# Optimization experiments

Hardware: AMD Instinct MI355X
Metric: run time of the kernel (lower is better)

Reference implementation:

```python
import jax, jax.numpy as jnp
import numpy as np

# ---- constants derived from configs / input sizes ----
H1, W1 = 480, 640
H2, W2 = 480, 640
WINDOW = 0.125      # normalized half-window (config['window_size'])
WG = 16             # window grid resolution per axis
L = 128             # samples along epipolar line (line_search_config)
T_BASE, T_MAX = 1.0, 50.0
NEG = -1e9


def l2norm(x, axis):
    return x / jnp.maximum(jnp.linalg.norm(x, axis=axis, keepdims=True), 1e-12)


def denorm(c_n, h, w):
    # normalized [-1,1] (xy) -> pixel coords, align_corners=True convention
    return jnp.stack([(c_n[..., 0] + 1) * (w - 1) / 2,
                      (c_n[..., 1] + 1) * (h - 1) / 2], -1)


def bilinear_sample(feat, coords_n):
    # feat [b,d,h,w], coords_n [b,n,2] in [-1,1] (xy); bilinear, zero padding
    b, d, h, w = feat.shape
    x = (coords_n[..., 0] + 1) * (w - 1) / 2
    y = (coords_n[..., 1] + 1) * (h - 1) / 2
    x0 = jnp.floor(x); y0 = jnp.floor(y)
    wx1 = x - x0; wx0 = 1 - wx1
    wy1 = y - y0; wy0 = 1 - wy1
    featT = feat.reshape(b, d, h * w).transpose(0, 2, 1)  # [b,hw,d]
    def gather(xi, yi, wgt):
        inb = (xi >= 0) & (xi <= w - 1) & (yi >= 0) & (yi <= h - 1)
        xi_ = jnp.clip(xi, 0, w - 1).astype(jnp.int32)
        yi_ = jnp.clip(yi, 0, h - 1).astype(jnp.int32)
        idx = yi_ * w + xi_
        v = jnp.take_along_axis(featT, idx[..., None], axis=1)  # [b,n,d]
        return v * (wgt * inb)[..., None]
    return (gather(x0, y0, wx0 * wy0) + gather(x0 + 1, y0, wx1 * wy0)
            + gather(x0, y0 + 1, wx0 * wy1) + gather(x0 + 1, y0 + 1, wx1 * wy1))


def soft_expect(corr, coords_n, valid):
    # corr [b,n,L], coords_n [b,n,L,2]; masked soft-argmax + std
    logits = jnp.where(valid, corr, NEG)
    p = jax.nn.softmax(logits, axis=-1)
    mean = jnp.einsum('bnl,bnlc->bnc', p, coords_n)
    var = jnp.einsum('bnl,bnlc->bnc', p, coords_n ** 2) - mean ** 2
    std = jnp.sqrt(jnp.clip(var, 0).sum(-1) + 1e-12)
    return mean, std, p


def epipolar_line_search(coord1_px, Fm, feat1, featmap2, h2, w2):
    # coord1_px [b,n,2] pixels in img1; Fm [b,3,3]; feat1 [b,n,d];
    # featmap2 [b,d,hf,wf] (already temperature * l2-normalized)
    b, n, _ = coord1_px.shape
    p1 = jnp.concatenate([coord1_px, jnp.ones_like(coord1_px[..., :1])], -1)
    line = jnp.einsum('bij,bnj->bni', Fm, p1)  # a x + b y + c = 0 in img2
    a, bb, c = line[..., 0], line[..., 1], line[..., 2]
    eps = 1e-8
    use_x = jnp.abs(bb) >= jnp.abs(a)  # near-horizontal line -> sweep x
    t = jnp.linspace(0.0, 1.0, L)
    xs_h = jnp.broadcast_to(t[None, None, :] * (w2 - 1), (b, n, L))
    ys_h = -(a[..., None] * xs_h + c[..., None]) / jnp.where(jnp.abs(bb) < eps, eps, bb)[..., None]
    ys_v = jnp.broadcast_to(t[None, None, :] * (h2 - 1), (b, n, L))
    xs_v = -(bb[..., None] * ys_v + c[..., None]) / jnp.where(jnp.abs(a) < eps, eps, a)[..., None]
    xs = jnp.where(use_x[..., None], xs_h, xs_v)
    ys = jnp.where(use_x[..., None], ys_h, ys_v)
    valid = (xs >= 0) & (xs <= w2 - 1) & (ys >= 0) & (ys <= h2 - 1)
    degen = (jnp.abs(a) < eps) & (jnp.abs(bb) < eps)
    valid = valid & (~degen[..., None])
    coords_n = jnp.stack([xs / ((w2 - 1) / 2) - 1, ys / ((h2 - 1) / 2) - 1], -1)
    feat_line = bilinear_sample(featmap2, coords_n.reshape(b, n * L, 2)).reshape(b, n, L, -1)
    corr = jnp.einsum('bnd,bnld->bnl', feat1, feat_line)
    mean, std, _ = soft_expect(corr, coords_n, valid)
    valid_kpt = valid.any(-1)
    clamped = jnp.clip(mean, -1 + WINDOW, 1 - WINDOW)  # window fits inside image
    return clamped, mean, valid_kpt, std


def window_expect(feat1, featmap2, center_n):
    b, n, _ = center_n.shape
    off = jnp.linspace(-WINDOW, WINDOW, WG)
    oy, ox = jnp.meshgrid(off, off, indexing='ij')
    offsets = jnp.stack([ox.ravel(), oy.ravel()], -1)            # [WG*WG,2]
    coords_n = center_n[:, :, None, :] + offsets[None, None]    # [b,n,K,2]
    K = WG * WG
    feat_w = bilinear_sample(featmap2, coords_n.reshape(b, n * K, 2)).reshape(b, n, K, -1)
    corr = jnp.einsum('bnd,bnkd->bnk', feat1, feat_w)
    valid = jnp.ones(corr.shape, bool)
    mean, std, p = soft_expect(corr, coords_n, valid)
    return mean, coords_n, std, p


def setup_inputs() -> dict:
    key = jax.random.key(0)
    ks = jax.random.split(key, 6)
    b, d, hf, wf, n = 2, 128, 60, 80, 1024
    xf1 = jax.random.normal(ks[0], (b, d, hf, wf), jnp.float32)
    xf2 = jax.random.normal(ks[1], (b, d, hf, wf), jnp.float32)
    # fundamental-matrix-like magnitudes so epipolar lines cross the image
    scale = jnp.array([[1e-5, 1e-5, 1e-2], [1e-5, 1e-5, 1e-2], [1e-2, 1e-2, 1.0]], jnp.float32)
    F1 = jax.random.normal(ks[2], (b, 3, 3), jnp.float32) * scale
    F2 = jax.random.normal(ks[3], (b, 3, 3), jnp.float32) * scale
    coord1_n = (jax.random.uniform(ks[4], (b, n, 2), jnp.float32) * 2 - 1) * 0.95
    coord2_n = (jax.random.uniform(ks[5], (b, n, 2), jnp.float32) * 2 - 1) * 0.95
    return {"xf1": xf1, "xf2": xf2, "F1": F1, "F2": F2,
            "coord1_n": coord1_n, "coord2_n": coord2_n, "epoch": 10}


def reference(xf1, xf2, F1, F2, coord1_n, coord2_n, epoch):
    temperature = jnp.minimum(jnp.float32(T_BASE + epoch), T_MAX)
    coord1 = denorm(coord1_n, H1, W1)
    coord2 = denorm(coord2_n, H2, W2)
    # loss_distance == 'cos' -> l2-normalize sampled descriptors
    feat1 = l2norm(bilinear_sample(xf1, coord1_n), -1)
    feat2 = l2norm(bilinear_sample(xf2, coord2_n), -1)
    fm2 = temperature * l2norm(xf2, 1)
    fm1 = temperature * l2norm(xf1, 1)
    c1_cl, c1_org_n, valid1, epi_std1 = epipolar_line_search(coord1, F1, feat1, fm2, H2, W2)
    c2_cl, c2_org_n, valid2, epi_std2 = epipolar_line_search(coord2, F2, feat2, fm1, H1, W1)
    feat1c_corloc_org = denorm(c1_org_n, H2, W2)
    f1w_n, _, f1w_std, _ = window_expect(feat1, fm2, c1_cl)
    f2w_n, _, f2w_std, _ = window_expect(feat2, fm1, c2_cl)
    feat1w_corloc = denorm(f1w_n, H2, W2)
    feat2w_corloc = denorm(f2w_n, H1, W1)
    # note: original (faithfully) returns the NORMALIZED coords for image-2 org key
    return (coord1, coord2, feat1w_corloc, feat2w_corloc,
            feat1c_corloc_org, c2_org_n, f1w_std, f2w_std, valid1, valid2)
```

## Files before the change

### kernel.cpp

```cpp
#include <hip/hip_runtime.h>
#include <stdint.h>

namespace {

typedef _Float16 half_t;
typedef _Float16 half2_t __attribute__((ext_vector_type(2)));

constexpr int D    = 128;
constexpr int WFm  = 80;
constexpr int HFm  = 60;
constexpr int NPIX = WFm * HFm;
constexpr int NKPT = 1024;
constexpr int LCX  = 12;
constexpr int LCY  = 10;
constexpr int NLAT = LCX * LCY;

__device__ __forceinline__ float wsum(float v) {
#pragma unroll
  for (int m = 32; m; m >>= 1) v += __shfl_xor(v, m, 64);
  return v;
}
__device__ __forceinline__ float wmax(float v) {
#pragma unroll
  for (int m = 32; m; m >>= 1) v = fmaxf(v, __shfl_xor(v, m, 64));
  return v;
}

__device__ __forceinline__ float dot2acc(uint32_t m, uint32_t f, float acc) {
#if defined(__has_builtin) && __has_builtin(__builtin_amdgcn_fdot2)
  return __builtin_amdgcn_fdot2(__builtin_bit_cast(half2_t, m),
                                __builtin_bit_cast(half2_t, f), acc, false);
#else
  half2_t a = __builtin_bit_cast(half2_t, m);
  half2_t b = __builtin_bit_cast(half2_t, f);
  return acc + (float)a.x * (float)b.x + (float)a.y * (float)b.y;
#endif
}
__device__ __forceinline__ float dot4x2(uint4 m, uint4 f, float acc) {
  acc = dot2acc(m.x, f.x, acc);
  acc = dot2acc(m.y, f.y, acc);
  acc = dot2acc(m.z, f.z, acc);
  acc = dot2acc(m.w, f.w, acc);
  return acc;
}

__global__ __launch_bounds__(256) void prep_kernel(
    const float* __restrict__ xf1, const float* __restrict__ xf2,
    const int* __restrict__ epoch,
    half_t* __restrict__ xf1H, half_t* __restrict__ xf2H,
    float* __restrict__ sc1, float* __restrict__ sc2) {
  __shared__ float tile[32 * 129];
  __shared__ float qSh[8][32];
  __shared__ float sSh[32];

  const int bi   = blockIdx.x;
  const int img  = bi / 300;
  const int rem  = bi % 300;
  const int b    = rem / 150;
  const int p0   = (rem % 150) * 32;
  const int tid  = threadIdx.x;

  const float* src  = img ? xf2 : xf1;
  half_t* dstH      = img ? xf2H : xf1H;
  float* dstS       = img ? sc2 : sc1;
  const float T     = fminf(1.0f + (float)(*epoch), 50.0f);

  const int dc = tid >> 5;
  const int px = tid & 31;
#pragma unroll 4
  for (int it = 0; it < 16; ++it) {
    int d = it * 8 + dc;
    tile[px * 129 + d] = src[((size_t)(b * D + d)) * NPIX + p0 + px];
  }
  __syncthreads();

  {
    float s = 0.f;
    const int d0 = dc * 16;
#pragma unroll 8
    for (int d = 0; d < 16; ++d) {
      float v = tile[px * 129 + d0 + d];
      s += v * v;
    }
    qSh[dc][px] = s;
  }
  __syncthreads();
  if (tid < 32) {
    float s = 0.f;
#pragma unroll
    for (int k = 0; k < 8; ++k) s += qSh[k][tid];
    float sv = T / fmaxf(sqrtf(s), 1e-12f);
    dstS[b * NPIX + p0 + tid] = sv;
    sSh[tid] = sv;
  }
  __syncthreads();

#pragma unroll 4
  for (int it = 0; it < 8; ++it) {
    int idx = it * 256 + tid;
    int lpx = idx >> 6;
    int dp  = idx & 63;
    float s = sSh[lpx];
    half2_t hv;
    hv.x = (half_t)(tile[lpx * 129 + 2 * dp] * s);
    hv.y = (half_t)(tile[lpx * 129 + 2 * dp + 1] * s);
    *reinterpret_cast<half2_t*>(dstH + ((size_t)(b * NPIX + p0 + lpx)) * D + 2 * dp) = hv;
  }
}

__global__ __launch_bounds__(256) void line2win_kernel(
    const half_t* __restrict__ xf1H, const half_t* __restrict__ xf2H,
    const float* __restrict__ sc1, const float* __restrict__ sc2,
    const float* __restrict__ F1, const float* __restrict__ F2,
    const float* __restrict__ c1n, const float* __restrict__ c2n,
    float* __restrict__ out) {
  __shared__ __align__(16) half_t featH[4][D];
  __shared__ float4 sPar[4][2][128];
  __shared__ float corrSh[4][128];
  __shared__ float dm[4][NLAT + 8];

  const int tid  = threadIdx.x;
  const int lane = tid & 63;
  const int wv   = tid >> 6;
  const int w    = blockIdx.x;
  const int xcd  = w & 7;
  const int comb = xcd >> 1;
  const int dir  = comb >> 1;
  const int b    = comb & 1;
  const int n    = ((w >> 3) * 2 + (xcd & 1)) * 4 + wv;
  const int kix  = b * NKPT + n;

  const half_t* srcH = dir ? xf2H : xf1H;
  const float*  ssc  = dir ? sc2 : sc1;
  const half_t* tgtH = dir ? xf1H : xf2H;
  const float*  Fm   = (dir ? F2 : F1) + b * 9;
  const float*  cn   = (dir ? c2n : c1n) + kix * 2;

  const float cnx_in = cn[0], cny_in = cn[1];
  const float px = (cnx_in + 1.f) * 319.5f;
  const float py = (cny_in + 1.f) * 239.5f;

  const float la = Fm[0] * px + Fm[1] * py + Fm[2];
  const float lb = Fm[3] * px + Fm[4] * py + Fm[5];
  const float lc = Fm[6] * px + Fm[7] * py + Fm[8];
  const float eps = 1e-8f;
  const bool  use_x = fabsf(lb) >= fabsf(la);
  const float bden  = (fabsf(lb) < eps) ? eps : lb;
  const float aden  = (fabsf(la) < eps) ? eps : la;
  const float rdenom = 1.f / (use_x ? bden : aden);
  const bool  degen = (fabsf(la) < eps) && (fabsf(lb) < eps);

  const size_t tb = (size_t)b * NPIX * D;

  float f0 = 0.f, f1 = 0.f;
  {
    float xf = (cnx_in + 1.f) * 39.5f;
    float yf = (cny_in + 1.f) * 29.5f;
    float x0 = floorf(xf), y0 = floorf(yf);
    float wx1 = xf - x0, wx0 = 1.f - wx1;
    float wy1 = yf - y0, wy0 = 1.f - wy1;
#pragma unroll
    for (int cyi = 0; cyi < 2; ++cyi)
#pragma unroll
      for (int cxi = 0; cxi < 2; ++cxi) {
        float xi = x0 + (float)cxi, yi = y0 + (float)cyi;
        bool inb = (xi >= 0.f) && (xi <= (float)(WFm - 1)) &&
                   (yi >= 0.f) && (yi <= (float)(HFm - 1));
        float wgt = (cxi ? wx1 : wx0) * (cyi ? wy1 : wy0);
        if (inb && wgt != 0.f) {
          int p = (int)yi * WFm + (int)xi;
          float coef = wgt / ssc[b * NPIX + p];
          half2_t hv = *reinterpret_cast<const half2_t*>(srcH + tb + (size_t)p * D + 2 * lane);
          f0 += coef * (float)hv.x;
          f1 += coef * (float)hv.y;
        }
      }
  }

#pragma unroll
  for (int q = 0; q < 2; ++q) {
    int j = lane + q * 64;
    float tpar = (float)j / 127.0f;
    float xs, ys;
    if (use_x) { xs = tpar * 639.f; ys = -fmaf(la, xs, lc) * rdenom; }
    else       { ys = tpar * 479.f; xs = -fmaf(lb, ys, lc) * rdenom; }
    float xff = fminf(fmaxf(xs * (39.5f / 319.5f), -4.f), 84.f);
    float yff = fminf(fmaxf(ys * (29.5f / 239.5f), -4.f), 64.f);
    float x0f = floorf(xff), y0f = floorf(yff);
    int  x0i = (int)x0f, y0i = (int)y0f;
    float wx1 = xff - x0f, wx0 = 1.f - wx1;
    float wy1 = yff - y0f;
    int  xLow = min(max(x0i, 0), WFm - 2);
    float cL0 = (xLow == x0i) ? wx0 : ((xLow == x0i + 1) ? wx1 : 0.f);
    float cH0 = (xLow + 1 == x0i) ? wx0 : ((xLow + 1 == x0i + 1) ? wx1 : 0.f);
#pragma unroll
    for (int h = 0; h < 2; ++h) {
      int yi = y0i + h;
      bool yin = (yi >= 0) && (yi <= HFm - 1);
      int yc = min(max(yi, 0), HFm - 1);
      float wyh = h ? wy1 : (1.f - wy1);
      float ymul = yin ? wyh : 0.f;
      float4 p4;
      p4.x = __int_as_float(yc * WFm + xLow);
      p4.y = cL0 * ymul;
      p4.z = cH0 * ymul;
      p4.w = 0.f;
      sPar[wv][h][j] = p4;
    }
  }

  const float nrm = wsum(f0 * f0 + f1 * f1);
  const float inv = 1.f / fmaxf(sqrtf(nrm), 1e-12f);
  {
    half2_t hv;
    hv.x = (half_t)(f0 * inv);
    hv.y = (half_t)(f1 * inv);
    *reinterpret_cast<half2_t*>(&featH[wv][2 * lane]) = hv;
  }

  const uint4* fH4 = reinterpret_cast<const uint4*>(featH[wv]);

  {
    const int g = lane >> 4;
    const int s = lane & 7;
    const int h = (lane >> 3) & 1;
    const uint4 fL0 = fH4[s];
    const uint4 fL1 = fH4[8 + s];

    float4 pA = sPar[wv][h][g];
    bool actA = (pA.y != 0.f) || (pA.z != 0.f);
    uint4 a0{}, a1{}, a2{}, a3{};
    if (actA) {
      const uint4* rp = reinterpret_cast<const uint4*>(
          tgtH + tb + (size_t)__float_as_int(pA.x) * D);
      a0 = rp[s]; a1 = rp[8 + s]; a2 = rp[16 + s]; a3 = rp[24 + s];
    }
    float4 pB = sPar[wv][h][4 + g];
    bool actB = (pB.y != 0.f) || (pB.z != 0.f);
    uint4 b0{}, b1{}, b2{}, b3{};
    if (actB) {
      const uint4* rp = reinterpret_cast<const uint4*>(
          tgtH + tb + (size_t)__float_as_int(pB.x) * D);
      b0 = rp[s]; b1 = rp[8 + s]; b2 = rp[16 + s]; b3 = rp[24 + s];
    }

#pragma unroll
    for (int it = 0; it < 32; ++it) {
      float4 pC = {0.f, 0.f, 0.f, 0.f};
      bool actC = false;
      uint4 c0{}, c1{}, c2{}, c3{};
      if (it < 30) {
        pC = sPar[wv][h][(it + 2) * 4 + g];
        actC = (pC.y != 0.f) || (pC.z != 0.f);
        if (actC) {
          const uint4* rp = reinterpret_cast<const uint4*>(
              tgtH + tb + (size_t)__float_as_int(pC.x) * D);
          c0 = rp[s]; c1 = rp[8 + s]; c2 = rp[16 + s]; c3 = rp[24 + s];
        }
      }
      float acc = 0.f;
      if (actA) {
        float accL = dot4x2(a1, fL1, dot4x2(a0, fL0, 0.f));
        float accH = dot4x2(a3, fL1, dot4x2(a2, fL0, 0.f));
        acc = pA.y * accL + pA.z * accH;
      }
      acc += __shfl_xor(acc, 1, 64);
      acc += __shfl_xor(acc, 2, 64);
      acc += __shfl_xor(acc, 4, 64);
      acc += __shfl_xor(acc, 8, 64);
      if ((lane & 15) == 0) corrSh[wv][it * 4 + g] = acc;
      pA = pB; actA = actB; a0 = b0; a1 = b1; a2 = b2; a3 = b3;
      pB = pC; actB = actC; b0 = c0; b1 = c1; b2 = c2; b3 = c3;
    }
  }

  float e0, e1, cx0, cy0, cx1, cy1;
  bool v0, v1;
  {
    float lgt0, lgt1;
#pragma unroll
    for (int q = 0; q < 2; ++q) {
      int j = lane + q * 64;
      float tpar = (float)j / 127.0f;
      float xs, ys;
      if (use_x) { xs = tpar * 639.f; ys = -fmaf(la, xs, lc) * rdenom; }
      else       { ys = tpar * 479.f; xs = -fmaf(lb, ys, lc) * rdenom; }
      bool valid = (xs >= 0.f) && (xs <= 639.f) && (ys >= 0.f) && (ys <= 479.f) && !degen;
      float cxj = xs / 319.5f - 1.f;
      float cyj = ys / 239.5f - 1.f;
      float lg = valid ? corrSh[wv][j] : -1e9f;
      if (q == 0) { v0 = valid; cx0 = cxj; cy0 = cyj; lgt0 = lg; }
      else        { v1 = valid; cx1 = cxj; cy1 = cyj; lgt1 = lg; }
    }
    const float mx = wmax(fmaxf(lgt0, lgt1));
    e0 = expf(lgt0 - mx);
    e1 = expf(lgt1 - mx);
  }
  const float sumE = wsum(e0 + e1);
  const float sumX = wsum(e0 * cx0 + e1 * cx1);
  const float sumY = wsum(e0 * cy0 + e1 * cy1);
  const bool  anyv = __ballot(v0 || v1) != 0ull;
  const float meanx = sumX / sumE;
  const float meany = sumY / sumE;
  const float ccx = fminf(fmaxf(meanx, -0.875f), 0.875f);
  const float ccy = fminf(fmaxf(meany, -0.875f), 0.875f);

  if (lane == 0) {
    float* o_coord = out + dir * 4096 + kix * 2;
    o_coord[0] = px;
    o_coord[1] = py;
    float* o_org = out + 16384 + dir * 4096 + kix * 2;
    if (dir == 0) {
      o_org[0] = (meanx + 1.f) * 319.5f;
      o_org[1] = (meany + 1.f) * 239.5f;
    } else {
      o_org[0] = meanx;
      o_org[1] = meany;
    }
    out[28672 + dir * 2048 + kix] = anyv ? 1.f : 0.f;
  }

  const float xfc2 = (ccx + 1.f) * 39.5f;
  const float yfc2 = (ccy + 1.f) * 29.5f;
  const int xb = (int)floorf(xfc2 - 4.9375f);
  const int yb = (int)floorf(yfc2 - 3.6875f);
  {
    const int s4 = lane & 15;
    const int pp = lane >> 4;
    const uint4 fw = fH4[s4];
    const int x0p = xb + pp, x1p = xb + 4 + pp, x2p = xb + 8 + pp;
    const bool okx0 = x0p <= WFm - 1, okx1 = x1p <= WFm - 1, okx2 = x2p <= WFm - 1;
    const int pc0 = min(x0p, WFm - 1) - xb;
    const int pc1 = min(x1p, WFm - 1) - xb;
    const int pc2 = min(x2p, WFm - 1) - xb;

    const uint4* rpA = reinterpret_cast<const uint4*>(
        tgtH + tb + (size_t)(min(yb, HFm - 1) * WFm + xb) * D);
    uint4 A0 = rpA[pc0 * 16 + s4];
    uint4 A1 = rpA[pc1 * 16 + s4];
    uint4 A2 = rpA[pc2 * 16 + s4];
#pragma unroll
    for (int row = 0; row < LCY; ++row) {
      uint4 B0{}, B1{}, B2{};
      if (row < LCY - 1) {
        int ycl = min(yb + row + 1, HFm - 1);
        const uint4* rpB = reinterpret_cast<const uint4*>(
            tgtH + tb + (size_t)(ycl * WFm + xb) * D);
        B0 = rpB[pc0 * 16 + s4];
        B1 = rpB[pc1 * 16 + s4];
        B2 = rpB[pc2 * 16 + s4];
      }
      bool yok = (yb + row) <= HFm - 1;
      float d0 = dot4x2(A0, fw, 0.f);
      float d1 = dot4x2(A1, fw, 0.f);
      float d2 = dot4x2(A2, fw, 0.f);
#pragma unroll
      for (int m = 1; m <= 8; m <<= 1) {
        d0 += __shfl_xor(d0, m, 64);
        d1 += __shfl_xor(d1, m, 64);
        d2 += __shfl_xor(d2, m, 64);
      }
      if (s4 == 0) {
        dm[wv][row * LCX + pp]     = (yok && okx0) ? d0 : 0.f;
        dm[wv][row * LCX + 4 + pp] = (yok && okx1) ? d1 : 0.f;
        dm[wv][row * LCX + 8 + pp] = (yok && okx2) ? d2 : 0.f;
      }
      A0 = B0; A1 = B1; A2 = B2;
    }
  }

  const float step = 0.25f / 15.f;
  float t0 = 0.f, t1 = 0.f, t2 = 0.f, t3 = 0.f, t4 = 0.f;
#pragma unroll
  for (int q = 0; q < 4; ++q) {
    int k = lane + q * 64;
    float ox = -0.125f + step * (float)(k & 15);
    float oy = -0.125f + step * (float)(k >> 4);
    float kcx = ccx + ox;
    float kcy = ccy + oy;
    float xfw = xfc2 + ox * 39.5f;
    float yfw = yfc2 + oy * 29.5f;
    float xw0 = floorf(xfw), yw0 = floorf(yfw);
    int ix = (int)xw0 - xb;
    int iy = (int)yw0 - yb;
    float wxx1 = xfw - xw0, wxx0 = 1.f - wxx1;
    float wyy1 = yfw - yw0, wyy0 = 1.f - wyy1;
    int i00 = iy * LCX + ix;
    float c00 = dm[wv][i00], c10 = dm[wv][i00 + 1];
    float c01 = dm[wv][i00 + LCX], c11 = dm[wv][i00 + LCX + 1];
    float corr2 = wxx0 * wyy0 * c00 + wxx1 * wyy0 * c10 +
                  wxx0 * wyy1 * c01 + wxx1 * wyy1 * c11;
    float e2 = expf(corr2);
    t0 += e2;
    t1 += e2 * kcx;
    t2 += e2 * kcy;
    t3 += e2 * kcx * kcx;
    t4 += e2 * kcy * kcy;
  }
  t0 = wsum(t0);
  t1 = wsum(t1);
  t2 = wsum(t2);
  t3 = wsum(t3);
  t4 = wsum(t4);
  if (lane == 0) {
    float mwx = t1 / t0;
    float mwy = t2 / t0;
    float vx  = fmaxf(t3 / t0 - mwx * mwx, 0.f);
    float vy  = fmaxf(t4 / t0 - mwy * mwy, 0.f);
    float stdv = sqrtf(vx + vy + 1e-12f);
    float* o_w = out + 8192 + dir * 4096 + kix * 2;
    o_w[0] = (mwx + 1.f) * 319.5f;
    o_w[1] = (mwy + 1.f) * 239.5f;
    out[24576 + dir * 2048 + kix] = stdv;
  }
}

}

extern "C" void kernel_launch(void* const* d_in, const int* in_sizes, int n_in,
                              void* d_out, int out_size, void* d_ws, size_t ws_size,
                              hipStream_t stream) {
  (void)in_sizes; (void)n_in; (void)out_size; (void)ws_size;
  const float* xf1 = (const float*)d_in[0];
  const float* xf2 = (const float*)d_in[1];
  const float* F1  = (const float*)d_in[2];
  const float* F2  = (const float*)d_in[3];
  const float* c1n = (const float*)d_in[4];
  const float* c2n = (const float*)d_in[5];
  const int* epoch = (const int*)d_in[6];

  half_t* xf1H = (half_t*)d_ws;
  half_t* xf2H = xf1H + (size_t)2 * NPIX * D;
  float*  sc1  = (float*)(xf2H + (size_t)2 * NPIX * D);
  float*  sc2  = sc1 + 2 * NPIX;
  float*  out  = (float*)d_out;

  hipLaunchKernelGGL(prep_kernel, dim3(600), dim3(256), 0, stream,
                     xf1, xf2, epoch, xf1H, xf2H, sc1, sc2);
  hipLaunchKernelGGL(line2win_kernel, dim3(1024), dim3(256), 0, stream,
                     xf1H, xf2H, sc1, sc2, F1, F2, c1n, c2n, out);
}
```

Baseline: 37.62 us.

## Split each keypoint's line and window search across two waves per block

Instead of one wavefront handling a whole keypoint (four keypoints per 256-thread block), each keypoint now gets a 128-thread block of two wavefronts. One wave samples and normalises the source descriptor while the other builds the line sample parameters. Both waves then share the 128 line correlations, the window rows and the window expectation samples, with partial sums combined through shared memory. This cuts the serial per-keypoint latency and launches four times as many blocks, at the cost of extra __syncthreads barriers and some duplicated softmax work in both waves.

```diff
diff --git a/kernel.cpp b/kernel.cpp
--- a/kernel.cpp
+++ b/kernel.cpp
@@ -108,26 +108,27 @@
   }
 }
 
-__global__ __launch_bounds__(256) void line2win_kernel(
+__global__ __launch_bounds__(128) void line2win_kernel(
     const half_t* __restrict__ xf1H, const half_t* __restrict__ xf2H,
     const float* __restrict__ sc1, const float* __restrict__ sc2,
     const float* __restrict__ F1, const float* __restrict__ F2,
     const float* __restrict__ c1n, const float* __restrict__ c2n,
     float* __restrict__ out) {
-  __shared__ __align__(16) half_t featH[4][D];
-  __shared__ float4 sPar[4][2][128];
-  __shared__ float corrSh[4][128];
-  __shared__ float dm[4][NLAT + 8];
+  __shared__ __align__(16) half_t featH[D];
+  __shared__ float4 sPar[2][128];
+  __shared__ float corrSh[128];
+  __shared__ float dm[NLAT + 8];
+  __shared__ float pT[2][5];
 
   const int tid  = threadIdx.x;
   const int lane = tid & 63;
-  const int wv   = tid >> 6;
+  const int wvh  = tid >> 6;
   const int w    = blockIdx.x;
   const int xcd  = w & 7;
   const int comb = xcd >> 1;
   const int dir  = comb >> 1;
   const int b    = comb & 1;
-  const int n    = ((w >> 3) * 2 + (xcd & 1)) * 4 + wv;
+  const int n    = (w >> 3) * 2 + (xcd & 1);
   const int kix  = b * NKPT + n;
 
   const half_t* srcH = dir ? xf2H : xf1H;
@@ -152,73 +153,73 @@
 
   const size_t tb = (size_t)b * NPIX * D;
 
-  float f0 = 0.f, f1 = 0.f;
-  {
-    float xf = (cnx_in + 1.f) * 39.5f;
-    float yf = (cny_in + 1.f) * 29.5f;
-    float x0 = floorf(xf), y0 = floorf(yf);
-    float wx1 = xf - x0, wx0 = 1.f - wx1;
-    float wy1 = yf - y0, wy0 = 1.f - wy1;
-#pragma unroll
-    for (int cyi = 0; cyi < 2; ++cyi)
-#pragma unroll
-      for (int cxi = 0; cxi < 2; ++cxi) {
-        float xi = x0 + (float)cxi, yi = y0 + (float)cyi;
-        bool inb = (xi >= 0.f) && (xi <= (float)(WFm - 1)) &&
-                   (yi >= 0.f) && (yi <= (float)(HFm - 1));
-        float wgt = (cxi ? wx1 : wx0) * (cyi ? wy1 : wy0);
-        if (inb && wgt != 0.f) {
-          int p = (int)yi * WFm + (int)xi;
-          float coef = wgt / ssc[b * NPIX + p];
-          half2_t hv = *reinterpret_cast<const half2_t*>(srcH + tb + (size_t)p * D + 2 * lane);
-          f0 += coef * (float)hv.x;
-          f1 += coef * (float)hv.y;
+  if (wvh == 0) {
+    float f0 = 0.f, f1 = 0.f;
+    {
+      float xf = (cnx_in + 1.f) * 39.5f;
+      float yf = (cny_in + 1.f) * 29.5f;
+      float x0 = floorf(xf), y0 = floorf(yf);
+      float wx1 = xf - x0, wx0 = 1.f - wx1;
+      float wy1 = yf - y0, wy0 = 1.f - wy1;
+#pragma unroll
+      for (int cyi = 0; cyi < 2; ++cyi)
+#pragma unroll
+        for (int cxi = 0; cxi < 2; ++cxi) {
+          float xi = x0 + (float)cxi, yi = y0 + (float)cyi;
+          bool inb = (xi >= 0.f) && (xi <= (float)(WFm - 1)) &&
+                     (yi >= 0.f) && (yi <= (float)(HFm - 1));
+          float wgt = (cxi ? wx1 : wx0) * (cyi ? wy1 : wy0);
+          if (inb && wgt != 0.f) {
+            int p = (int)yi * WFm + (int)xi;
+            float coef = wgt / ssc[b * NPIX + p];
+            half2_t hv = *reinterpret_cast<const half2_t*>(srcH + tb + (size_t)p * D + 2 * lane);
+            f0 += coef * (float)hv.x;
+            f1 += coef * (float)hv.y;
+          }
         }
-      }
-  }
-
-#pragma unroll
-  for (int q = 0; q < 2; ++q) {
-    int j = lane + q * 64;
-    float tpar = (float)j / 127.0f;
-    float xs, ys;
-    if (use_x) { xs = tpar * 639.f; ys = -fmaf(la, xs, lc) * rdenom; }
-    else       { ys = tpar * 479.f; xs = -fmaf(lb, ys, lc) * rdenom; }
-    float xff = fminf(fmaxf(xs * (39.5f / 319.5f), -4.f), 84.f);
-    float yff = fminf(fmaxf(ys * (29.5f / 239.5f), -4.f), 64.f);
-    float x0f = floorf(xff), y0f = floorf(yff);
-    int  x0i = (int)x0f, y0i = (int)y0f;
-    float wx1 = xff - x0f, wx0 = 1.f - wx1;
-    float wy1 = yff - y0f;
-    int  xLow = min(max(x0i, 0), WFm - 2);
-    float cL0 = (xLow == x0i) ? wx0 : ((xLow == x0i + 1) ? wx1 : 0.f);
-    float cH0 = (xLow + 1 == x0i) ? wx0 : ((xLow + 1 == x0i + 1) ? wx1 : 0.f);
-#pragma unroll
-    for (int h = 0; h < 2; ++h) {
-      int yi = y0i + h;
-      bool yin = (yi >= 0) && (yi <= HFm - 1);
-      int yc = min(max(yi, 0), HFm - 1);
-      float wyh = h ? wy1 : (1.f - wy1);
-      float ymul = yin ? wyh : 0.f;
-      float4 p4;
-      p4.x = __int_as_float(yc * WFm + xLow);
-      p4.y = cL0 * ymul;
-      p4.z = cH0 * ymul;
-      p4.w = 0.f;
-      sPar[wv][h][j] = p4;
-    }
-  }
-
-  const float nrm = wsum(f0 * f0 + f1 * f1);
-  const float inv = 1.f / fmaxf(sqrtf(nrm), 1e-12f);
-  {
+    }
+    const float nrm = wsum(f0 * f0 + f1 * f1);
+    const float inv = 1.f / fmaxf(sqrtf(nrm), 1e-12f);
     half2_t hv;
     hv.x = (half_t)(f0 * inv);
     hv.y = (half_t)(f1 * inv);
-    *reinterpret_cast<half2_t*>(&featH[wv][2 * lane]) = hv;
-  }
-
-  const uint4* fH4 = reinterpret_cast<const uint4*>(featH[wv]);
+    *reinterpret_cast<half2_t*>(&featH[2 * lane]) = hv;
+  } else {
+#pragma unroll
+    for (int q = 0; q < 2; ++q) {
+      int j = lane + q * 64;
+      float tpar = (float)j / 127.0f;
+      float xs, ys;
+      if (use_x) { xs = tpar * 639.f; ys = -fmaf(la, xs, lc) * rdenom; }
+      else       { ys = tpar * 479.f; xs = -fmaf(lb, ys, lc) * rdenom; }
+      float xff = fminf(fmaxf(xs * (39.5f / 319.5f), -4.f), 84.f);
+      float yff = fminf(fmaxf(ys * (29.5f / 239.5f), -4.f), 64.f);
+      float x0f = floorf(xff), y0f = floorf(yff);
+      int  x0i = (int)x0f, y0i = (int)y0f;
+      float wx1 = xff - x0f, wx0 = 1.f - wx1;
+      float wy1 = yff - y0f;
+      int  xLow = min(max(x0i, 0), WFm - 2);
+      float cL0 = (xLow == x0i) ? wx0 : ((xLow == x0i + 1) ? wx1 : 0.f);
+      float cH0 = (xLow + 1 == x0i) ? wx0 : ((xLow + 1 == x0i + 1) ? wx1 : 0.f);
+#pragma unroll
+      for (int h = 0; h < 2; ++h) {
+        int yi = y0i + h;
+        bool yin = (yi >= 0) && (yi <= HFm - 1);
+        int yc = min(max(yi, 0), HFm - 1);
+        float wyh = h ? wy1 : (1.f - wy1);
+        float ymul = yin ? wyh : 0.f;
+        float4 p4;
+        p4.x = __int_as_float(yc * WFm + xLow);
+        p4.y = cL0 * ymul;
+        p4.z = cH0 * ymul;
+        p4.w = 0.f;
+        sPar[h][j] = p4;
+      }
+    }
+  }
+  __syncthreads();
+
+  const uint4* fH4 = reinterpret_cast<const uint4*>(featH);
 
   {
     const int g = lane >> 4;
@@ -226,8 +227,9 @@
     const int h = (lane >> 3) & 1;
     const uint4 fL0 = fH4[s];
     const uint4 fL1 = fH4[8 + s];
-
-    float4 pA = sPar[wv][h][g];
+    const int jb = wvh * 64 + g;
+
+    float4 pA = sPar[h][jb];
     bool actA = (pA.y != 0.f) || (pA.z != 0.f);
     uint4 a0{}, a1{}, a2{}, a3{};
     if (actA) {
@@ -235,7 +237,7 @@
           tgtH + tb + (size_t)__float_as_int(pA.x) * D);
       a0 = rp[s]; a1 = rp[8 + s]; a2 = rp[16 + s]; a3 = rp[24 + s];
     }
-    float4 pB = sPar[wv][h][4 + g];
+    float4 pB = sPar[h][jb + 4];
     bool actB = (pB.y != 0.f) || (pB.z != 0.f);
     uint4 b0{}, b1{}, b2{}, b3{};
     if (actB) {
@@ -245,12 +247,12 @@
     }
 
 #pragma unroll
-    for (int it = 0; it < 32; ++it) {
+    for (int rt = 0; rt < 16; ++rt) {
       float4 pC = {0.f, 0.f, 0.f, 0.f};
       bool actC = false;
       uint4 c0{}, c1{}, c2{}, c3{};
-      if (it < 30) {
-        pC = sPar[wv][h][(it + 2) * 4 + g];
+      if (rt < 14) {
+        pC = sPar[h][jb + (rt + 2) * 4];
         actC = (pC.y != 0.f) || (pC.z != 0.f);
         if (actC) {
           const uint4* rp = reinterpret_cast<const uint4*>(
@@ -268,11 +270,12 @@
       acc += __shfl_xor(acc, 2, 64);
       acc += __shfl_xor(acc, 4, 64);
       acc += __shfl_xor(acc, 8, 64);
-      if ((lane & 15) == 0) corrSh[wv][it * 4 + g] = acc;
+      if ((lane & 15) == 0) corrSh[jb + rt * 4] = acc;
       pA = pB; actA = actB; a0 = b0; a1 = b1; a2 = b2; a3 = b3;
       pB = pC; actB = actC; b0 = c0; b1 = c1; b2 = c2; b3 = c3;
     }
   }
+  __syncthreads();
 
   float e0, e1, cx0, cy0, cx1, cy1;
   bool v0, v1;
@@ -288,7 +291,7 @@
       bool valid = (xs >= 0.f) && (xs <= 639.f) && (ys >= 0.f) && (ys <= 479.f) && !degen;
       float cxj = xs / 319.5f - 1.f;
       float cyj = ys / 239.5f - 1.f;
-      float lg = valid ? corrSh[wv][j] : -1e9f;
+      float lg = valid ? corrSh[j] : -1e9f;
       if (q == 0) { v0 = valid; cx0 = cxj; cy0 = cyj; lgt0 = lg; }
       else        { v1 = valid; cx1 = cxj; cy1 = cyj; lgt1 = lg; }
     }
@@ -305,7 +308,7 @@
   const float ccx = fminf(fmaxf(meanx, -0.875f), 0.875f);
   const float ccy = fminf(fmaxf(meany, -0.875f), 0.875f);
 
-  if (lane == 0) {
+  if (tid == 0) {
     float* o_coord = out + dir * 4096 + kix * 2;
     o_coord[0] = px;
     o_coord[1] = py;
@@ -335,15 +338,16 @@
     const int pc2 = min(x2p, WFm - 1) - xb;
 
     const uint4* rpA = reinterpret_cast<const uint4*>(
-        tgtH + tb + (size_t)(min(yb, HFm - 1) * WFm + xb) * D);
+        tgtH + tb + (size_t)(min(yb + wvh, HFm - 1) * WFm + xb) * D);
     uint4 A0 = rpA[pc0 * 16 + s4];
     uint4 A1 = rpA[pc1 * 16 + s4];
     uint4 A2 = rpA[pc2 * 16 + s4];
 #pragma unroll
-    for (int row = 0; row < LCY; ++row) {
+    for (int r8 = 0; r8 < 5; ++r8) {
+      const int row = wvh + 2 * r8;
       uint4 B0{}, B1{}, B2{};
-      if (row < LCY - 1) {
-        int ycl = min(yb + row + 1, HFm - 1);
+      if (r8 < 4) {
+        int ycl = min(yb + row + 2, HFm - 1);
         const uint4* rpB = reinterpret_cast<const uint4*>(
             tgtH + tb + (size_t)(ycl * WFm + xb) * D);
         B0 = rpB[pc0 * 16 + s4];
@@ -361,19 +365,20 @@
         d2 += __shfl_xor(d2, m, 64);
       }
       if (s4 == 0) {
-        dm[wv][row * LCX + pp]     = (yok && okx0) ? d0 : 0.f;
-        dm[wv][row * LCX + 4 + pp] = (yok && okx1) ? d1 : 0.f;
-        dm[wv][row * LCX + 8 + pp] = (yok && okx2) ? d2 : 0.f;
+        dm[row * LCX + pp]     = (yok && okx0) ? d0 : 0.f;
+        dm[row * LCX + 4 + pp] = (yok && okx1) ? d1 : 0.f;
+        dm[row * LCX + 8 + pp] = (yok && okx2) ? d2 : 0.f;
       }
       A0 = B0; A1 = B1; A2 = B2;
     }
   }
+  __syncthreads();
 
   const float step = 0.25f / 15.f;
   float t0 = 0.f, t1 = 0.f, t2 = 0.f, t3 = 0.f, t4 = 0.f;
 #pragma unroll
-  for (int q = 0; q < 4; ++q) {
-    int k = lane + q * 64;
+  for (int qq = 0; qq < 2; ++qq) {
+    int k = lane + (wvh * 2 + qq) * 64;
     float ox = -0.125f + step * (float)(k & 15);
     float oy = -0.125f + step * (float)(k >> 4);
     float kcx = ccx + ox;
@@ -386,8 +391,8 @@
     float wxx1 = xfw - xw0, wxx0 = 1.f - wxx1;
     float wyy1 = yfw - yw0, wyy0 = 1.f - wyy1;
     int i00 = iy * LCX + ix;
-    float c00 = dm[wv][i00], c10 = dm[wv][i00 + 1];
-    float c01 = dm[wv][i00 + LCX], c11 = dm[wv][i00 + LCX + 1];
+    float c00 = dm[i00], c10 = dm[i00 + 1];
+    float c01 = dm[i00 + LCX], c11 = dm[i00 + LCX + 1];
     float corr2 = wxx0 * wyy0 * c00 + wxx1 * wyy0 * c10 +
                   wxx0 * wyy1 * c01 + wxx1 * wyy1 * c11;
     float e2 = expf(corr2);
@@ -403,10 +408,20 @@
   t3 = wsum(t3);
   t4 = wsum(t4);
   if (lane == 0) {
-    float mwx = t1 / t0;
-    float mwy = t2 / t0;
-    float vx  = fmaxf(t3 / t0 - mwx * mwx, 0.f);
-    float vy  = fmaxf(t4 / t0 - mwy * mwy, 0.f);
+    pT[wvh][0] = t0; pT[wvh][1] = t1; pT[wvh][2] = t2;
+    pT[wvh][3] = t3; pT[wvh][4] = t4;
+  }
+  __syncthreads();
+  if (tid == 0) {
+    float s0 = pT[0][0] + pT[1][0];
+    float s1 = pT[0][1] + pT[1][1];
+    float s2 = pT[0][2] + pT[1][2];
+    float s3 = pT[0][3] + pT[1][3];
+    float s4 = pT[0][4] + pT[1][4];
+    float mwx = s1 / s0;
+    float mwy = s2 / s0;
+    float vx  = fmaxf(s3 / s0 - mwx * mwx, 0.f);
+    float vy  = fmaxf(s4 / s0 - mwy * mwy, 0.f);
     float stdv = sqrtf(vx + vy + 1e-12f);
     float* o_w = out + 8192 + dir * 4096 + kix * 2;
     o_w[0] = (mwx + 1.f) * 319.5f;
@@ -437,6 +452,6 @@
 
   hipLaunchKernelGGL(prep_kernel, dim3(600), dim3(256), 0, stream,
                      xf1, xf2, epoch, xf1H, xf2H, sc1, sc2);
-  hipLaunchKernelGGL(line2win_kernel, dim3(1024), dim3(256), 0, stream,
+  hipLaunchKernelGGL(line2win_kernel, dim3(4096), dim3(128), 0, stream,
                      xf1H, xf2H, sc1, sc2, F1, F2, c1n, c2n, out);
 }
```

Result: slower. 40.55 us (+7.8%).

## Split line search into one-wave blocks and vectorize prep loads and stores

Applied to the files above, without the earlier changes.

The line/window kernel now launches 4096 single-wavefront blocks instead of 1024 four-wave blocks, with per-wave shared arrays collapsed to a single instance. This gives the scheduler finer-grained work units and may improve load balance across CUs. The prep kernel now reads float2 pairs from the channel-major input and writes 8-byte packed half4 stores, using a padded 32x130 tile. Wider memory transactions should cut instruction count, but the new tile stride may change LDS bank-conflict behaviour.

```diff
diff --git a/kernel.cpp b/kernel.cpp
--- a/kernel.cpp
+++ b/kernel.cpp
@@ -49,7 +49,7 @@
     const int* __restrict__ epoch,
     half_t* __restrict__ xf1H, half_t* __restrict__ xf2H,
     float* __restrict__ sc1, float* __restrict__ sc2) {
-  __shared__ float tile[32 * 129];
+  __shared__ float tile[32][130];
   __shared__ float qSh[8][32];
   __shared__ float sSh[32];
 
@@ -65,24 +65,28 @@
   float* dstS       = img ? sc2 : sc1;
   const float T     = fminf(1.0f + (float)(*epoch), 50.0f);
 
-  const int dc = tid >> 5;
-  const int px = tid & 31;
-#pragma unroll 4
-  for (int it = 0; it < 16; ++it) {
-    int d = it * 8 + dc;
-    tile[px * 129 + d] = src[((size_t)(b * D + d)) * NPIX + p0 + px];
+  const int dc  = tid >> 4;
+  const int pxp = tid & 15;
+#pragma unroll
+  for (int it = 0; it < 8; ++it) {
+    int d = it * 16 + dc;
+    float2 v = *reinterpret_cast<const float2*>(
+        &src[((size_t)(b * D + d)) * NPIX + p0 + 2 * pxp]);
+    tile[2 * pxp][d]     = v.x;
+    tile[2 * pxp + 1][d] = v.y;
   }
   __syncthreads();
 
   {
+    const int px = tid & 31;
+    const int dg = tid >> 5;
     float s = 0.f;
-    const int d0 = dc * 16;
-#pragma unroll 8
+#pragma unroll
     for (int d = 0; d < 16; ++d) {
-      float v = tile[px * 129 + d0 + d];
+      float v = tile[px][dg * 16 + d];
       s += v * v;
     }
-    qSh[dc][px] = s;
+    qSh[dg][px] = s;
   }
   __syncthreads();
   if (tid < 32) {
@@ -95,39 +99,42 @@
   }
   __syncthreads();
 
-#pragma unroll 4
-  for (int it = 0; it < 8; ++it) {
+#pragma unroll
+  for (int it = 0; it < 4; ++it) {
     int idx = it * 256 + tid;
-    int lpx = idx >> 6;
-    int dp  = idx & 63;
+    int lpx = idx >> 5;
+    int dq  = (idx & 31) * 4;
     float s = sSh[lpx];
-    half2_t hv;
-    hv.x = (half_t)(tile[lpx * 129 + 2 * dp] * s);
-    hv.y = (half_t)(tile[lpx * 129 + 2 * dp + 1] * s);
-    *reinterpret_cast<half2_t*>(dstH + ((size_t)(b * NPIX + p0 + lpx)) * D + 2 * dp) = hv;
-  }
-}
-
-__global__ __launch_bounds__(256) void line2win_kernel(
+    half2_t h0, h1;
+    h0.x = (half_t)(tile[lpx][dq] * s);
+    h0.y = (half_t)(tile[lpx][dq + 1] * s);
+    h1.x = (half_t)(tile[lpx][dq + 2] * s);
+    h1.y = (half_t)(tile[lpx][dq + 3] * s);
+    uint2 pack;
+    pack.x = __builtin_bit_cast(uint32_t, h0);
+    pack.y = __builtin_bit_cast(uint32_t, h1);
+    *reinterpret_cast<uint2*>(dstH + ((size_t)(b * NPIX + p0 + lpx)) * D + dq) = pack;
+  }
+}
+
+__global__ __launch_bounds__(64) void line2win_kernel(
     const half_t* __restrict__ xf1H, const half_t* __restrict__ xf2H,
     const float* __restrict__ sc1, const float* __restrict__ sc2,
     const float* __restrict__ F1, const float* __restrict__ F2,
     const float* __restrict__ c1n, const float* __restrict__ c2n,
     float* __restrict__ out) {
-  __shared__ __align__(16) half_t featH[4][D];
-  __shared__ float4 sPar[4][2][128];
-  __shared__ float corrSh[4][128];
-  __shared__ float dm[4][NLAT + 8];
-
-  const int tid  = threadIdx.x;
-  const int lane = tid & 63;
-  const int wv   = tid >> 6;
+  __shared__ __align__(16) half_t featH[D];
+  __shared__ float4 sPar[2][128];
+  __shared__ float corrSh[128];
+  __shared__ float dm[NLAT + 8];
+
+  const int lane = threadIdx.x;
   const int w    = blockIdx.x;
   const int xcd  = w & 7;
   const int comb = xcd >> 1;
   const int dir  = comb >> 1;
   const int b    = comb & 1;
-  const int n    = ((w >> 3) * 2 + (xcd & 1)) * 4 + wv;
+  const int n    = (w >> 3) * 2 + (xcd & 1);
   const int kix  = b * NKPT + n;
 
   const half_t* srcH = dir ? xf2H : xf1H;
@@ -205,7 +212,7 @@
       p4.y = cL0 * ymul;
       p4.z = cH0 * ymul;
       p4.w = 0.f;
-      sPar[wv][h][j] = p4;
+      sPar[h][j] = p4;
     }
   }
 
@@ -215,10 +222,10 @@
     half2_t hv;
     hv.x = (half_t)(f0 * inv);
     hv.y = (half_t)(f1 * inv);
-    *reinterpret_cast<half2_t*>(&featH[wv][2 * lane]) = hv;
-  }
-
-  const uint4* fH4 = reinterpret_cast<const uint4*>(featH[wv]);
+    *reinterpret_cast<half2_t*>(&featH[2 * lane]) = hv;
+  }
+
+  const uint4* fH4 = reinterpret_cast<const uint4*>(featH);
 
   {
     const int g = lane >> 4;
@@ -227,7 +234,7 @@
     const uint4 fL0 = fH4[s];
     const uint4 fL1 = fH4[8 + s];
 
-    float4 pA = sPar[wv][h][g];
+    float4 pA = sPar[h][g];
     bool actA = (pA.y != 0.f) || (pA.z != 0.f);
     uint4 a0{}, a1{}, a2{}, a3{};
     if (actA) {
@@ -235,7 +242,7 @@
           tgtH + tb + (size_t)__float_as_int(pA.x) * D);
       a0 = rp[s]; a1 = rp[8 + s]; a2 = rp[16 + s]; a3 = rp[24 + s];
     }
-    float4 pB = sPar[wv][h][4 + g];
+    float4 pB = sPar[h][4 + g];
     bool actB = (pB.y != 0.f) || (pB.z != 0.f);
     uint4 b0{}, b1{}, b2{}, b3{};
     if (actB) {
@@ -250,7 +257,7 @@
       bool actC = false;
       uint4 c0{}, c1{}, c2{}, c3{};
       if (it < 30) {
-        pC = sPar[wv][h][(it + 2) * 4 + g];
+        pC = sPar[h][(it + 2) * 4 + g];
         actC = (pC.y != 0.f) || (pC.z != 0.f);
         if (actC) {
           const uint4* rp = reinterpret_cast<const uint4*>(
@@ -268,7 +275,7 @@
       acc += __shfl_xor(acc, 2, 64);
       acc += __shfl_xor(acc, 4, 64);
       acc += __shfl_xor(acc, 8, 64);
-      if ((lane & 15) == 0) corrSh[wv][it * 4 + g] = acc;
+      if ((lane & 15) == 0) corrSh[it * 4 + g] = acc;
       pA = pB; actA = actB; a0 = b0; a1 = b1; a2 = b2; a3 = b3;
       pB = pC; actB = actC; b0 = c0; b1 = c1; b2 = c2; b3 = c3;
     }
@@ -288,7 +295,7 @@
       bool valid = (xs >= 0.f) && (xs <= 639.f) && (ys >= 0.f) && (ys <= 479.f) && !degen;
       float cxj = xs / 319.5f - 1.f;
       float cyj = ys / 239.5f - 1.f;
-      float lg = valid ? corrSh[wv][j] : -1e9f;
+      float lg = valid ? corrSh[j] : -1e9f;
       if (q == 0) { v0 = valid; cx0 = cxj; cy0 = cyj; lgt0 = lg; }
       else        { v1 = valid; cx1 = cxj; cy1 = cyj; lgt1 = lg; }
     }
@@ -361,9 +368,9 @@
         d2 += __shfl_xor(d2, m, 64);
       }
       if (s4 == 0) {
-        dm[wv][row * LCX + pp]     = (yok && okx0) ? d0 : 0.f;
-        dm[wv][row * LCX + 4 + pp] = (yok && okx1) ? d1 : 0.f;
-        dm[wv][row * LCX + 8 + pp] = (yok && okx2) ? d2 : 0.f;
+        dm[row * LCX + pp]     = (yok && okx0) ? d0 : 0.f;
+        dm[row * LCX + 4 + pp] = (yok && okx1) ? d1 : 0.f;
+        dm[row * LCX + 8 + pp] = (yok && okx2) ? d2 : 0.f;
       }
       A0 = B0; A1 = B1; A2 = B2;
     }
@@ -386,8 +393,8 @@
     float wxx1 = xfw - xw0, wxx0 = 1.f - wxx1;
     float wyy1 = yfw - yw0, wyy0 = 1.f - wyy1;
     int i00 = iy * LCX + ix;
-    float c00 = dm[wv][i00], c10 = dm[wv][i00 + 1];
-    float c01 = dm[wv][i00 + LCX], c11 = dm[wv][i00 + LCX + 1];
+    float c00 = dm[i00], c10 = dm[i00 + 1];
+    float c01 = dm[i00 + LCX], c11 = dm[i00 + LCX + 1];
     float corr2 = wxx0 * wyy0 * c00 + wxx1 * wyy0 * c10 +
                   wxx0 * wyy1 * c01 + wxx1 * wyy1 * c11;
     float e2 = expf(corr2);
@@ -437,6 +444,6 @@
 
   hipLaunchKernelGGL(prep_kernel, dim3(600), dim3(256), 0, stream,
                      xf1, xf2, epoch, xf1H, xf2H, sc1, sc2);
-  hipLaunchKernelGGL(line2win_kernel, dim3(1024), dim3(256), 0, stream,
+  hipLaunchKernelGGL(line2win_kernel, dim3(4096), dim3(64), 0, stream,
                      xf1H, xf2H, sc1, sc2, F1, F2, c1n, c2n, out);
 }
```

Measured after the change: 37.31 us. Within noise of the previous version (-0.8%).
